# Performance work log

Hardware: AMD Instinct MI355X
Metric: run time of the kernel (lower is better)

## Reference

```python
import jax, jax.numpy as jnp
import numpy as np

H, D = 8, 16
HID = H * D  # 128 hidden channels
NU, NI = 20000, 50000
E_UI, E_IU, E_UU = 250000, 250000, 125000


def _agg(scores, vals, dst, n):
    # segment softmax over incoming edges per dst node, then scatter-add.
    # scores: [E, H], vals: [E, H, D], dst: [E]
    m = jax.ops.segment_max(scores, dst, num_segments=n)
    m = jnp.where(jnp.isfinite(m), m, 0.0)
    e = jnp.exp(scores - m[dst])
    den = jax.ops.segment_sum(e, dst, num_segments=n) + 1e-16
    alpha = e / den[dst]
    return jax.ops.segment_sum(vals * alpha[..., None], dst, num_segments=n)


def setup_inputs() -> dict:
    key = jax.random.key(0)
    ks = iter(jax.random.split(key, 40))
    def nrm(shape, scale):
        return jax.random.normal(next(ks), shape, dtype=jnp.float32) * scale
    L = 2
    inp = {}
    inp['x_user'] = nrm((NU, 128), 1.0)
    inp['x_item'] = nrm((NI, 64), 1.0)
    inp['edge_src_ui'] = jax.random.randint(next(ks), (E_UI,), 0, NU, dtype=jnp.int32)
    inp['edge_dst_ui'] = jax.random.randint(next(ks), (E_UI,), 0, NI, dtype=jnp.int32)
    inp['edge_src_iu'] = jax.random.randint(next(ks), (E_IU,), 0, NI, dtype=jnp.int32)
    inp['edge_dst_iu'] = jax.random.randint(next(ks), (E_IU,), 0, NU, dtype=jnp.int32)
    inp['edge_src_uu'] = jax.random.randint(next(ks), (E_UU,), 0, NU, dtype=jnp.int32)
    inp['edge_dst_uu'] = jax.random.randint(next(ks), (E_UU,), 0, NU, dtype=jnp.int32)
    inp['W_in_user'] = nrm((128, HID), 128 ** -0.5)
    inp['b_in_user'] = jnp.zeros((HID,), jnp.float32)
    inp['W_in_item'] = nrm((64, HID), 64 ** -0.5)
    inp['b_in_item'] = jnp.zeros((HID,), jnp.float32)
    inp['W_kqv_user'] = nrm((L, HID, 3 * HID), HID ** -0.5)
    inp['b_kqv_user'] = jnp.zeros((L, 3 * HID), jnp.float32)
    inp['W_kqv_item'] = nrm((L, HID, 3 * HID), HID ** -0.5)
    inp['b_kqv_item'] = jnp.zeros((L, 3 * HID), jnp.float32)
    inp['W_out_user'] = nrm((L, HID, HID), HID ** -0.5)
    inp['b_out_user'] = jnp.zeros((L, HID), jnp.float32)
    inp['W_out_item'] = nrm((L, HID, HID), HID ** -0.5)
    inp['b_out_item'] = jnp.zeros((L, HID), jnp.float32)
    inp['skip_user'] = jnp.ones((L,), jnp.float32)
    inp['skip_item'] = jnp.ones((L,), jnp.float32)
    inp['A_k'] = nrm((L, 3, H, D, D), D ** -0.5)
    inp['A_v'] = nrm((L, 3, H, D, D), D ** -0.5)
    inp['p_rel'] = jnp.ones((L, 3, H), jnp.float32)
    inp['W_lin'] = nrm((HID, 64), HID ** -0.5)
    inp['b_lin'] = jnp.zeros((64,), jnp.float32)
    return inp


def reference(x_user, x_item, edge_src_ui, edge_dst_ui, edge_src_iu, edge_dst_iu,
              edge_src_uu, edge_dst_uu, W_in_user, b_in_user, W_in_item, b_in_item,
              W_kqv_user, b_kqv_user, W_kqv_item, b_kqv_item, W_out_user, b_out_user,
              W_out_item, b_out_item, skip_user, skip_item, A_k, A_v, p_rel,
              W_lin, b_lin):
    inv_sqrt_d = 1.0 / jnp.sqrt(jnp.float32(D))
    # per-node-type input projection + relu
    xu = jax.nn.relu(x_user @ W_in_user + b_in_user)  # [NU, HID]
    xi = jax.nn.relu(x_item @ W_in_item + b_in_item)  # [NI, HID]
    L = W_kqv_user.shape[0]
    for l in range(L):
        kqv_u = xu @ W_kqv_user[l] + b_kqv_user[l]
        k_u, q_u, v_u = [t.reshape(-1, H, D) for t in jnp.split(kqv_u, 3, axis=1)]
        kqv_i = xi @ W_kqv_item[l] + b_kqv_item[l]
        k_i, q_i, v_i = [t.reshape(-1, H, D) for t in jnp.split(kqv_i, 3, axis=1)]

        def edge_msgs(k_src, v_src, q_dst, src, dst, r):
            # relation-specific key/value transforms, gathered per edge
            ke = jnp.einsum('ehd,hdf->ehf', k_src[src], A_k[l, r])  # [E,H,D]
            ve = jnp.einsum('ehd,hdf->ehf', v_src[src], A_v[l, r])  # [E,H,D]
            sc = (q_dst[dst] * ke).sum(-1) * p_rel[l, r] * inv_sqrt_d  # [E,H]
            return sc, ve

        s_ui, m_ui = edge_msgs(k_u, v_u, q_i, edge_src_ui, edge_dst_ui, 0)
        s_iu, m_iu = edge_msgs(k_i, v_i, q_u, edge_src_iu, edge_dst_iu, 1)
        s_uu, m_uu = edge_msgs(k_u, v_u, q_u, edge_src_uu, edge_dst_uu, 2)

        out_i = _agg(s_ui, m_ui, edge_dst_ui, NI).reshape(NI, HID)
        out_u = _agg(jnp.concatenate([s_iu, s_uu]),
                     jnp.concatenate([m_iu, m_uu]),
                     jnp.concatenate([edge_dst_iu, edge_dst_uu]), NU).reshape(NU, HID)

        # gelu -> per-type output linear -> sigmoid-gated skip (PyG HGTConv)
        a_u = jax.nn.gelu(out_u, approximate=False) @ W_out_user[l] + b_out_user[l]
        a_i = jax.nn.gelu(out_i, approximate=False) @ W_out_item[l] + b_out_item[l]
        g_u = jax.nn.sigmoid(skip_user[l])
        g_i = jax.nn.sigmoid(skip_item[l])
        xu = jax.nn.relu(g_u * a_u + (1.0 - g_u) * xu)
        xi = jax.nn.relu(g_i * a_i + (1.0 - g_i) * xi)
    # shared final linear over both node types; concat user then item rows
    out = jnp.concatenate([xu, xi], axis=0) @ W_lin + b_lin  # [NU+NI, 64]
    return out
```

## Files before the change

kernel.cpp:

```cpp
#include <hip/hip_runtime.h>
#include <math.h>

namespace {

constexpr int kNU  = 20000;
constexpr int kNI  = 50000;
constexpr int kEUI = 250000;
constexpr int kEIU = 250000;
constexpr int kEUU = 125000;
constexpr int kEU  = kEIU + kEUU;

typedef __attribute__((ext_vector_type(8))) short bf16x8_t;
typedef __attribute__((ext_vector_type(4))) float f32x4_t;

__device__ __forceinline__ float geluf(float x) {
  return 0.5f * x * (1.0f + erff(x * 0.7071067811865475f));
}

__device__ __forceinline__ void split_bf16(float x, unsigned short& hi, unsigned short& lo) {
  unsigned u = __float_as_uint(x);
  unsigned h = (u + 0x7FFFu + ((u >> 16) & 1u)) >> 16;
  hi = (unsigned short)h;
  float r = x - __uint_as_float(h << 16);
  unsigned ur = __float_as_uint(r);
  lo = (unsigned short)((ur + 0x7FFFu + ((ur >> 16) & 1u)) >> 16);
}

template <int ACT_IN, int EPI>
__global__ __launch_bounds__(256, 2) void mfma_gemm(
    const float* __restrict__ A, const unsigned short* __restrict__ Bt,
    const float* __restrict__ bias, float* C,
    int M, int N, int K,
    const float* x_old, const float* __restrict__ skip_scalar)
{
  __shared__ unsigned short sA[2][128][72];
  __shared__ unsigned short sB[2][128][72];
  const int tid = threadIdx.x;
  const int m0 = blockIdx.y * 128, n0 = blockIdx.x * 128;
  const int lane = tid & 63, w = tid >> 6;
  const int wm = w >> 1, wn = w & 1;
  const int fr = lane & 15, kg = lane >> 4;
  const unsigned short* Blo = Bt + (size_t)N * K;
  const int r = tid >> 1, seg = tid & 1;
  f32x4_t acc[4][4] = {};

  for (int k0 = 0; k0 < K; k0 += 64) {
    {
      const int arow = m0 + r;
      const bool am = arow < M;
      const float* ap = A + (size_t)arow * K + k0 + seg * 32;
      #pragma unroll
      for (int q = 0; q < 8; ++q) {
        float4 a = am ? *reinterpret_cast<const float4*>(ap + q * 4)
                      : make_float4(0.f, 0.f, 0.f, 0.f);
        if (ACT_IN == 1) { a.x = geluf(a.x); a.y = geluf(a.y); a.z = geluf(a.z); a.w = geluf(a.w); }
        ushort4 h, l;
        split_bf16(a.x, h.x, l.x); split_bf16(a.y, h.y, l.y);
        split_bf16(a.z, h.z, l.z); split_bf16(a.w, h.w, l.w);
        *reinterpret_cast<ushort4*>(&sA[0][r][seg * 32 + q * 4]) = h;
        *reinterpret_cast<ushort4*>(&sA[1][r][seg * 32 + q * 4]) = l;
      }
    }
    {
      const int brow = n0 + r;
      const bool bm = brow < N;
      const unsigned short* bh = Bt  + (size_t)brow * K + k0 + seg * 32;
      const unsigned short* bl = Blo + (size_t)brow * K + k0 + seg * 32;
      #pragma unroll
      for (int q = 0; q < 4; ++q) {
        uint4 vh = bm ? *reinterpret_cast<const uint4*>(bh + q * 8) : make_uint4(0, 0, 0, 0);
        uint4 vl = bm ? *reinterpret_cast<const uint4*>(bl + q * 8) : make_uint4(0, 0, 0, 0);
        *reinterpret_cast<uint4*>(&sB[0][r][seg * 32 + q * 8]) = vh;
        *reinterpret_cast<uint4*>(&sB[1][r][seg * 32 + q * 8]) = vl;
      }
    }
    __syncthreads();
    #pragma unroll
    for (int ks = 0; ks < 2; ++ks) {
      const int kb = ks * 32 + kg * 8;
      bf16x8_t ah[4], al[4], bh[4], bl[4];
      #pragma unroll
      for (int fm = 0; fm < 4; ++fm) {
        const int row = wm * 64 + fm * 16 + fr;
        ah[fm] = *reinterpret_cast<const bf16x8_t*>(&sA[0][row][kb]);
        al[fm] = *reinterpret_cast<const bf16x8_t*>(&sA[1][row][kb]);
      }
      #pragma unroll
      for (int fn = 0; fn < 4; ++fn) {
        const int row = wn * 64 + fn * 16 + fr;
        bh[fn] = *reinterpret_cast<const bf16x8_t*>(&sB[0][row][kb]);
        bl[fn] = *reinterpret_cast<const bf16x8_t*>(&sB[1][row][kb]);
      }
      #pragma unroll
      for (int fm = 0; fm < 4; ++fm)
        #pragma unroll
        for (int fn = 0; fn < 4; ++fn) {
          acc[fm][fn] = __builtin_amdgcn_mfma_f32_16x16x32_bf16(ah[fm], bh[fn], acc[fm][fn], 0, 0, 0);
          acc[fm][fn] = __builtin_amdgcn_mfma_f32_16x16x32_bf16(ah[fm], bl[fn], acc[fm][fn], 0, 0, 0);
          acc[fm][fn] = __builtin_amdgcn_mfma_f32_16x16x32_bf16(al[fm], bh[fn], acc[fm][fn], 0, 0, 0);
        }
    }
    __syncthreads();
  }

  float g = 0.f;
  if (EPI == 2) g = 1.f / (1.f + __expf(-skip_scalar[0]));
  #pragma unroll
  for (int fn = 0; fn < 4; ++fn) {
    const int col = n0 + wn * 64 + fn * 16 + fr;
    if (col >= N) continue;
    const float bv = bias[col];
    #pragma unroll
    for (int fm = 0; fm < 4; ++fm) {
      #pragma unroll
      for (int i = 0; i < 4; ++i) {
        const int row = m0 + wm * 64 + fm * 16 + kg * 4 + i;
        if (row >= M) continue;
        float v = acc[fm][fn][i] + bv;
        if (EPI == 1) v = fmaxf(v, 0.f);
        if (EPI == 2) {
          float xo = x_old[(size_t)row * 128 + col];
          v = fmaxf(g * v + (1.f - g) * xo, 0.f);
        }
        C[(size_t)row * N + col] = v;
      }
    }
  }
}

constexpr int kSlices = 16;

__device__ void conv_wt(const float* __restrict__ src, int ld, int cofs,
                        int Kd, int Nd, unsigned short* __restrict__ dst, int slice) {
  const int tot = Kd * Nd;
  for (int t = slice * 256 + threadIdx.x; t < tot; t += kSlices * 256) {
    const int n = t / Kd, k = t - n * Kd;
    unsigned short h, l;
    split_bf16(src[(size_t)k * ld + cofs + n], h, l);
    dst[t] = h; dst[tot + t] = l;
  }
}

__global__ __launch_bounds__(256) void build_weights(
    const float* __restrict__ Wku, const float* __restrict__ bku,
    const float* __restrict__ Wki, const float* __restrict__ bki,
    const float* __restrict__ A_k, const float* __restrict__ A_v,
    const float* __restrict__ p_rel,
    const float* __restrict__ W_in_u, const float* __restrict__ W_in_i,
    const float* __restrict__ W_out_u, const float* __restrict__ W_out_i,
    const float* __restrict__ W_lin,
    unsigned short* __restrict__ TWuU, unsigned short* __restrict__ TWiU,
    unsigned short* __restrict__ TWuI, unsigned short* __restrict__ TWqi,
    unsigned short* __restrict__ TWinU, unsigned short* __restrict__ TWinI,
    unsigned short* __restrict__ TWoutU, unsigned short* __restrict__ TWoutI,
    unsigned short* __restrict__ TWlin,
    float* __restrict__ buU, float* __restrict__ biU, float* __restrict__ buI)
{
  const int idx = blockIdx.x >> 4;
  const int slice = blockIdx.x & 15;
  if (idx < 12) {
    const int kv = idx & 1;
    const int lr = idx >> 1;
    const int l = lr / 3, r = lr - 3 * l;
    const float* A = (kv ? A_v : A_k) + (size_t)lr * 2048;
    const float* Wsrc = (r == 1) ? (Wki + (size_t)l * 128 * 384) : (Wku + (size_t)l * 128 * 384);
    const float* bsrc = (r == 1) ? (bki + (size_t)l * 384) : (bku + (size_t)l * 384);
    const int colsrc = kv ? 256 : 0;
    unsigned short* T; float* b; int colofs, Ntot;
    if (r == 2)      { T = TWuU + (size_t)l * 2 * 384 * 128; b = buU + l * 384; colofs = 128 + kv * 128; Ntot = 384; }
    else if (r == 1) { T = TWiU + (size_t)l * 2 * 256 * 128; b = biU + l * 256; colofs = kv * 128; Ntot = 256; }
    else             { T = TWuI + (size_t)l * 2 * 256 * 128; b = buI + l * 256; colofs = kv * 128; Ntot = 256; }
    __shared__ float sA[2048];
    for (int i = threadIdx.x; i < 2048; i += 256) sA[i] = A[i];
    __syncthreads();
    const int plane = Ntot * 128;
    for (int t = slice * 256 + threadIdx.x; t < 16384; t += kSlices * 256) {
      const int c = t >> 7, hf = t & 127, h = hf >> 4, f = hf & 15;
      const float scale = kv ? 1.f : p_rel[lr * 8 + h] * 0.25f;
      const float* wrow = Wsrc + (size_t)c * 384 + colsrc + h * 16;
      float s = 0.f;
      #pragma unroll
      for (int d = 0; d < 16; ++d) s += wrow[d] * sA[h * 256 + d * 16 + f];
      unsigned short hi, lo;
      split_bf16(s * scale, hi, lo);
      T[(size_t)(colofs + hf) * 128 + c] = hi;
      T[plane + (size_t)(colofs + hf) * 128 + c] = lo;
    }
    if (slice == 0) {
      for (int t = threadIdx.x; t < 128; t += 256) {
        const int h = t >> 4, f = t & 15;
        const float scale = kv ? 1.f : p_rel[lr * 8 + h] * 0.25f;
        float s = 0.f;
        #pragma unroll
        for (int d = 0; d < 16; ++d) s += bsrc[colsrc + h * 16 + d] * sA[h * 256 + d * 16 + f];
        b[colofs + t] = s * scale;
      }
    }
    return;
  }
  if (idx < 14) {
    const int l = idx - 12;
    const float* src = Wku + (size_t)l * 128 * 384;
    unsigned short* T = TWuU + (size_t)l * 2 * 384 * 128;
    const int plane = 384 * 128;
    for (int t = slice * 256 + threadIdx.x; t < 16384; t += kSlices * 256) {
      const int n = t >> 7, k = t & 127;
      unsigned short h, lo;
      split_bf16(src[(size_t)k * 384 + 128 + n], h, lo);
      T[(size_t)n * 128 + k] = h;
      T[plane + (size_t)n * 128 + k] = lo;
    }
    if (slice == 0)
      for (int t = threadIdx.x; t < 128; t += 256)
        buU[l * 384 + t] = bku[(size_t)l * 384 + 128 + t];
    return;
  }
  if (idx < 16) { conv_wt(Wki + (size_t)(idx - 14) * 128 * 384, 384, 128, 128, 128,
                          TWqi + (size_t)(idx - 14) * 2 * 128 * 128, slice); return; }
  if (idx == 16) { conv_wt(W_in_u, 128, 0, 128, 128, TWinU, slice); return; }
  if (idx == 17) { conv_wt(W_in_i, 128, 0, 64, 128, TWinI, slice); return; }
  if (idx < 20) { conv_wt(W_out_u + (size_t)(idx - 18) * 16384, 128, 0, 128, 128,
                          TWoutU + (size_t)(idx - 18) * 2 * 16384, slice); return; }
  if (idx < 22) { conv_wt(W_out_i + (size_t)(idx - 20) * 16384, 128, 0, 128, 128,
                          TWoutI + (size_t)(idx - 20) * 2 * 16384, slice); return; }
  conv_wt(W_lin, 64, 0, 128, 64, TWlin, slice);
}

__global__ void zero2_kernel(int* a, int na, int* b, int nb) {
  int i = blockIdx.x * 256 + threadIdx.x;
  if (i < na) a[i] = 0;
  if (i < nb) b[i] = 0;
}
__global__ void count_all(const int* __restrict__ dst_ui, const int* __restrict__ dst_iu,
                          const int* __restrict__ dst_uu,
                          int* __restrict__ cnt_i, int* __restrict__ cnt_u) {
  int e = blockIdx.x * 256 + threadIdx.x;
  if (e < kEUI) atomicAdd(&cnt_i[dst_ui[e]], 1);
  if (e < kEU) {
    int d = (e < kEIU) ? dst_iu[e] : dst_uu[e - kEIU];
    atomicAdd(&cnt_u[d], 1);
  }
}
__global__ void scatter_all(const int* __restrict__ dst_ui, const int* __restrict__ src_ui,
                            const int* __restrict__ dst_iu, const int* __restrict__ src_iu,
                            const int* __restrict__ dst_uu, const int* __restrict__ src_uu,
                            int* __restrict__ cur_i, int* __restrict__ list_i,
                            int* __restrict__ cur_u, int* __restrict__ list_u) {
  int e = blockIdx.x * 256 + threadIdx.x;
  if (e < kEUI) { int pos = atomicAdd(&cur_i[dst_ui[e]], 1); list_i[pos] = src_ui[e]; }
  if (e < kEU) {
    int d, sv;
    if (e < kEIU) { d = dst_iu[e]; sv = src_iu[e]; }
    else          { d = dst_uu[e - kEIU]; sv = src_uu[e - kEIU] | (int)0x80000000; }
    int pos = atomicAdd(&cur_u[d], 1);
    list_u[pos] = sv;
  }
}

__device__ void scan_body(const int* cnt_in, int* starts, int* cursor, int n) {
  __shared__ int wsum[16];
  __shared__ int s_carry;
  const int tid = threadIdx.x;
  const int lane = tid & 63, wv = tid >> 6;
  if (tid == 0) s_carry = 0;
  __syncthreads();
  for (int base = 0; base < n; base += 1024) {
    int i = base + tid;
    int v = (i < n) ? cnt_in[i] : 0;
    int s = v;
    #pragma unroll
    for (int off = 1; off < 64; off <<= 1) {
      int t = __shfl_up(s, off, 64);
      if (lane >= off) s += t;
    }
    if (lane == 63) wsum[wv] = s;
    __syncthreads();
    int woff = 0, total = 0;
    #pragma unroll
    for (int w = 0; w < 16; ++w) { total += wsum[w]; woff += (w < wv) ? wsum[w] : 0; }
    int excl = s_carry + woff + s - v;
    if (i < n) { starts[i] = excl; cursor[i] = excl; }
    __syncthreads();
    if (tid == 0) s_carry += total;
    __syncthreads();
  }
  if (tid == 0) starts[n] = s_carry;
}
__global__ __launch_bounds__(1024) void scan2_kernel(
    int* cnt_i, int* starts_i, int n_i, int* cnt_u, int* starts_u, int n_u) {
  if (blockIdx.x == 0) scan_body(cnt_i, starts_i, cnt_i, n_i);
  else                 scan_body(cnt_u, starts_u, cnt_u, n_u);
}

__global__ __launch_bounds__(256) void agg_wave_kernel(
    const int* __restrict__ starts, const int* __restrict__ list,
    const float* __restrict__ q, int qstride,
    const float* __restrict__ tabA, int strideA,
    const float* __restrict__ tabB, int strideB, int offB,
    float* __restrict__ out, int n_dst)
{
  const int dst = (int)((blockIdx.x * 256 + threadIdx.x) >> 6);
  if (dst >= n_dst) return;
  const int lane = threadIdx.x & 63;
  const int cofs = 2 * lane;
  const float2 qv = *reinterpret_cast<const float2*>(q + (size_t)dst * qstride + cofs);
  float m = -INFINITY, den = 0.f, a0 = 0.f, a1 = 0.f;
  const int i0 = starts[dst], i1 = starts[dst + 1];
  if (i0 < i1) {
    auto resolve = [&](int sv) -> const float* {
      return (sv < 0) ? tabB + (size_t)(sv & 0x7fffffff) * strideB + offB
                      : tabA + (size_t)sv * strideA;
    };
    int sv_n = list[i0];
    int sv_nn = (i0 + 1 < i1) ? list[i0 + 1] : 0;
    const float* kb = resolve(sv_n);
    float2 kk = *reinterpret_cast<const float2*>(kb + cofs);
    float2 vv = *reinterpret_cast<const float2*>(kb + 128 + cofs);
    for (int idx = i0; idx < i1; ++idx) {
      const float2 kc = kk, vc = vv;
      const int sv_next = sv_nn;
      if (idx + 2 < i1) sv_nn = list[idx + 2];
      if (idx + 1 < i1) {
        const float* kbn = resolve(sv_next);
        kk = *reinterpret_cast<const float2*>(kbn + cofs);
        vv = *reinterpret_cast<const float2*>(kbn + 128 + cofs);
      }
      float p = qv.x * kc.x + qv.y * kc.y;
      p += __shfl_xor(p, 1);
      p += __shfl_xor(p, 2);
      p += __shfl_xor(p, 4);
      const float mn = fmaxf(m, p);
      const float r  = __expf(m - mn);
      const float pe = __expf(p - mn);
      den = den * r + pe;
      a0  = a0 * r + pe * vc.x;
      a1  = a1 * r + pe * vc.y;
      m = mn;
    }
  }
  const float inv = 1.f / (den + 1e-16f);
  *reinterpret_cast<float2*>(out + (size_t)dst * 128 + cofs) = make_float2(a0 * inv, a1 * inv);
}

inline int cdiv(int a, int b) { return (a + b - 1) / b; }

}

extern "C" void kernel_launch(void* const* d_in, const int* in_sizes, int n_in,
                              void* d_out, int out_size, void* d_ws, size_t ws_size,
                              hipStream_t stream) {
  const float* x_user      = (const float*)d_in[0];
  const float* x_item      = (const float*)d_in[1];
  const int*   src_ui      = (const int*)d_in[2];
  const int*   dst_ui      = (const int*)d_in[3];
  const int*   src_iu      = (const int*)d_in[4];
  const int*   dst_iu      = (const int*)d_in[5];
  const int*   src_uu      = (const int*)d_in[6];
  const int*   dst_uu      = (const int*)d_in[7];
  const float* W_in_user   = (const float*)d_in[8];
  const float* b_in_user   = (const float*)d_in[9];
  const float* W_in_item   = (const float*)d_in[10];
  const float* b_in_item   = (const float*)d_in[11];
  const float* W_kqv_user  = (const float*)d_in[12];
  const float* b_kqv_user  = (const float*)d_in[13];
  const float* W_kqv_item  = (const float*)d_in[14];
  const float* b_kqv_item  = (const float*)d_in[15];
  const float* W_out_user  = (const float*)d_in[16];
  const float* b_out_user  = (const float*)d_in[17];
  const float* W_out_item  = (const float*)d_in[18];
  const float* b_out_item  = (const float*)d_in[19];
  const float* skip_user   = (const float*)d_in[20];
  const float* skip_item   = (const float*)d_in[21];
  const float* A_k         = (const float*)d_in[22];
  const float* A_v         = (const float*)d_in[23];
  const float* p_rel       = (const float*)d_in[24];
  const float* W_lin       = (const float*)d_in[25];
  const float* b_lin       = (const float*)d_in[26];
  float* out = (float*)d_out;
  (void)in_sizes; (void)n_in; (void)out_size; (void)ws_size;

  char* base = (char*)d_ws;
  size_t off = 0;
  auto alloc = [&](size_t nbytes) -> void* {
    void* p = base + off;
    off += (nbytes + 255) & ~(size_t)255;
    return p;
  };
  float* xu    = (float*)alloc((size_t)kNU * 128 * 4);
  float* xi    = (float*)alloc((size_t)kNI * 128 * 4);
  float* tab   = (float*)alloc((size_t)20480000 * 4);
  float* agg_u = (float*)alloc((size_t)kNU * 128 * 4);
  unsigned short* TWuU   = (unsigned short*)alloc((size_t)2 * 2 * 384 * 128 * 2);
  unsigned short* TWiU   = (unsigned short*)alloc((size_t)2 * 2 * 256 * 128 * 2);
  unsigned short* TWuI   = (unsigned short*)alloc((size_t)2 * 2 * 256 * 128 * 2);
  unsigned short* TWqi   = (unsigned short*)alloc((size_t)2 * 2 * 128 * 128 * 2);
  unsigned short* TWinU  = (unsigned short*)alloc((size_t)2 * 128 * 128 * 2);
  unsigned short* TWinI  = (unsigned short*)alloc((size_t)2 * 128 * 64 * 2);
  unsigned short* TWoutU = (unsigned short*)alloc((size_t)2 * 2 * 128 * 128 * 2);
  unsigned short* TWoutI = (unsigned short*)alloc((size_t)2 * 2 * 128 * 128 * 2);
  unsigned short* TWlin  = (unsigned short*)alloc((size_t)2 * 64 * 128 * 2);
  float* buU   = (float*)alloc((size_t)2 * 384 * 4);
  float* biU   = (float*)alloc((size_t)2 * 256 * 4);
  float* buI   = (float*)alloc((size_t)2 * 256 * 4);
  int* starts_i = (int*)alloc((size_t)(kNI + 1) * 4);
  int* cursor_i = (int*)alloc((size_t)kNI * 4);
  int* list_i   = (int*)alloc((size_t)kEUI * 4);
  int* starts_u = (int*)alloc((size_t)(kNU + 1) * 4);
  int* cursor_u = (int*)alloc((size_t)kNU * 4);
  int* list_u   = (int*)alloc((size_t)kEU * 4);

  float* u_all = tab + 0;
  float* i_all = tab + 7680000;
  float* u2    = tab + 0;
  float* q_i   = tab + 5120000;
  float* agg_i = tab + 11520000;

  zero2_kernel<<<cdiv(kNI, 256), 256, 0, stream>>>(cursor_i, kNI, cursor_u, kNU);
  count_all<<<cdiv(kEU, 256), 256, 0, stream>>>(dst_ui, dst_iu, dst_uu, cursor_i, cursor_u);
  scan2_kernel<<<2, 1024, 0, stream>>>(cursor_i, starts_i, kNI, cursor_u, starts_u, kNU);
  scatter_all<<<cdiv(kEU, 256), 256, 0, stream>>>(dst_ui, src_ui, dst_iu, src_iu,
                                                  dst_uu, src_uu, cursor_i, list_i,
                                                  cursor_u, list_u);

  build_weights<<<23 * kSlices, 256, 0, stream>>>(
      W_kqv_user, b_kqv_user, W_kqv_item, b_kqv_item, A_k, A_v, p_rel,
      W_in_user, W_in_item, W_out_user, W_out_item, W_lin,
      TWuU, TWiU, TWuI, TWqi, TWinU, TWinI, TWoutU, TWoutI, TWlin,
      buU, biU, buI);

  mfma_gemm<0, 1><<<dim3(1, cdiv(kNU, 128)), 256, 0, stream>>>(
      x_user, TWinU, b_in_user, xu, kNU, 128, 128, nullptr, nullptr);
  mfma_gemm<0, 1><<<dim3(1, cdiv(kNI, 128)), 256, 0, stream>>>(
      x_item, TWinI, b_in_item, xi, kNI, 128, 64, nullptr, nullptr);

  for (int l = 0; l < 2; ++l) {
    mfma_gemm<0, 0><<<dim3(3, cdiv(kNU, 128)), 256, 0, stream>>>(
        xu, TWuU + (size_t)l * 2 * 384 * 128, buU + l * 384, u_all, kNU, 384, 128,
        nullptr, nullptr);
    mfma_gemm<0, 0><<<dim3(2, cdiv(kNI, 128)), 256, 0, stream>>>(
        xi, TWiU + (size_t)l * 2 * 256 * 128, biU + l * 256, i_all, kNI, 256, 128,
        nullptr, nullptr);
    agg_wave_kernel<<<cdiv(kNU * 64, 256), 256, 0, stream>>>(
        starts_u, list_u, u_all, 384, i_all, 256, u_all, 384, 128, agg_u, kNU);

    mfma_gemm<0, 0><<<dim3(2, cdiv(kNU, 128)), 256, 0, stream>>>(
        xu, TWuI + (size_t)l * 2 * 256 * 128, buI + l * 256, u2, kNU, 256, 128,
        nullptr, nullptr);
    mfma_gemm<0, 0><<<dim3(1, cdiv(kNI, 128)), 256, 0, stream>>>(
        xi, TWqi + (size_t)l * 2 * 128 * 128, b_kqv_item + (size_t)l * 384 + 128,
        q_i, kNI, 128, 128, nullptr, nullptr);
    agg_wave_kernel<<<cdiv(kNI * 64, 256), 256, 0, stream>>>(
        starts_i, list_i, q_i, 128, u2, 256, u2, 256, 0, agg_i, kNI);

    mfma_gemm<1, 2><<<dim3(1, cdiv(kNU, 128)), 256, 0, stream>>>(
        agg_u, TWoutU + (size_t)l * 2 * 128 * 128, b_out_user + (size_t)l * 128,
        xu, kNU, 128, 128, xu, skip_user + l);
    mfma_gemm<1, 2><<<dim3(1, cdiv(kNI, 128)), 256, 0, stream>>>(
        agg_i, TWoutI + (size_t)l * 2 * 128 * 128, b_out_item + (size_t)l * 128,
        xi, kNI, 128, 128, xi, skip_item + l);
  }

  mfma_gemm<0, 0><<<dim3(1, cdiv(kNU + kNI, 128)), 256, 0, stream>>>(
      xu, TWlin, b_lin, out, kNU + kNI, 64, 128, nullptr, nullptr);
}
```

Before: 875.9 us.

## Store gathered key/value tables in fp16 and simplify aggregation loop

The GEMMs that produce per-edge key and value projections now write them as fp16 into packed tables, while query columns stay fp32. The aggregation kernel gathers half-precision k/v, halving the bytes per random gather, and converts to float for the online softmax. The software prefetch of the next row's k/v is removed in favour of a simpler loop that only prefetches the next index. Workspace layout is reshuffled to fit the smaller tables. The risks are fp16 rounding and range limits on k/v, and more exposed gather latency without the prefetch.

Measured after the change: 819.0 us. 6.5% less time.

```diff
diff --git a/kernel.cpp b/kernel.cpp
--- a/kernel.cpp
+++ b/kernel.cpp
@@ -12,6 +12,8 @@
 
 typedef __attribute__((ext_vector_type(8))) short bf16x8_t;
 typedef __attribute__((ext_vector_type(4))) float f32x4_t;
+
+struct h2v { _Float16 x, y; };
 
 __device__ __forceinline__ float geluf(float x) {
   return 0.5f * x * (1.0f + erff(x * 0.7071067811865475f));
@@ -26,12 +28,13 @@
   lo = (unsigned short)((ur + 0x7FFFu + ((ur >> 16) & 1u)) >> 16);
 }
 
-template <int ACT_IN, int EPI>
+template <int ACT_IN, int EPI, int OUT>
 __global__ __launch_bounds__(256, 2) void mfma_gemm(
     const float* __restrict__ A, const unsigned short* __restrict__ Bt,
     const float* __restrict__ bias, float* C,
     int M, int N, int K,
-    const float* x_old, const float* __restrict__ skip_scalar)
+    const float* x_old, const float* __restrict__ skip_scalar,
+    _Float16* __restrict__ Ckv, int qcols)
 {
   __shared__ unsigned short sA[2][128][72];
   __shared__ unsigned short sB[2][128][72];
@@ -105,6 +108,7 @@
 
   float g = 0.f;
   if (EPI == 2) g = 1.f / (1.f + __expf(-skip_scalar[0]));
+  const int kvN = (OUT == 1) ? (N - qcols) : 0;
   #pragma unroll
   for (int fn = 0; fn < 4; ++fn) {
     const int col = n0 + wn * 64 + fn * 16 + fr;
@@ -122,7 +126,12 @@
           float xo = x_old[(size_t)row * 128 + col];
           v = fmaxf(g * v + (1.f - g) * xo, 0.f);
         }
-        C[(size_t)row * N + col] = v;
+        if (OUT == 0) {
+          C[(size_t)row * N + col] = v;
+        } else {
+          if (col < qcols) C[(size_t)row * qcols + col] = v;
+          else             Ckv[(size_t)row * kvN + (col - qcols)] = (_Float16)v;
+        }
       }
     }
   }
@@ -294,49 +303,37 @@
 
 __global__ __launch_bounds__(256) void agg_wave_kernel(
     const int* __restrict__ starts, const int* __restrict__ list,
-    const float* __restrict__ q, int qstride,
-    const float* __restrict__ tabA, int strideA,
-    const float* __restrict__ tabB, int strideB, int offB,
+    const float* __restrict__ q,
+    const _Float16* __restrict__ tabA, const _Float16* __restrict__ tabB,
     float* __restrict__ out, int n_dst)
 {
   const int dst = (int)((blockIdx.x * 256 + threadIdx.x) >> 6);
   if (dst >= n_dst) return;
   const int lane = threadIdx.x & 63;
   const int cofs = 2 * lane;
-  const float2 qv = *reinterpret_cast<const float2*>(q + (size_t)dst * qstride + cofs);
+  const float2 qv = *reinterpret_cast<const float2*>(q + (size_t)dst * 128 + cofs);
   float m = -INFINITY, den = 0.f, a0 = 0.f, a1 = 0.f;
-  const int i0 = starts[dst], i1 = starts[dst + 1];
-  if (i0 < i1) {
-    auto resolve = [&](int sv) -> const float* {
-      return (sv < 0) ? tabB + (size_t)(sv & 0x7fffffff) * strideB + offB
-                      : tabA + (size_t)sv * strideA;
-    };
-    int sv_n = list[i0];
-    int sv_nn = (i0 + 1 < i1) ? list[i0 + 1] : 0;
-    const float* kb = resolve(sv_n);
-    float2 kk = *reinterpret_cast<const float2*>(kb + cofs);
-    float2 vv = *reinterpret_cast<const float2*>(kb + 128 + cofs);
-    for (int idx = i0; idx < i1; ++idx) {
-      const float2 kc = kk, vc = vv;
-      const int sv_next = sv_nn;
-      if (idx + 2 < i1) sv_nn = list[idx + 2];
-      if (idx + 1 < i1) {
-        const float* kbn = resolve(sv_next);
-        kk = *reinterpret_cast<const float2*>(kbn + cofs);
-        vv = *reinterpret_cast<const float2*>(kbn + 128 + cofs);
-      }
-      float p = qv.x * kc.x + qv.y * kc.y;
-      p += __shfl_xor(p, 1);
-      p += __shfl_xor(p, 2);
-      p += __shfl_xor(p, 4);
-      const float mn = fmaxf(m, p);
-      const float r  = __expf(m - mn);
-      const float pe = __expf(p - mn);
-      den = den * r + pe;
-      a0  = a0 * r + pe * vc.x;
-      a1  = a1 * r + pe * vc.y;
-      m = mn;
-    }
+  const int i1 = starts[dst + 1];
+  int idx = starts[dst];
+  int sv_next = (idx < i1) ? list[idx] : 0;
+  for (; idx < i1; ++idx) {
+    const int sv = sv_next;
+    if (idx + 1 < i1) sv_next = list[idx + 1];
+    const _Float16* kb = (sv < 0) ? tabB + (size_t)(sv & 0x7fffffff) * 256
+                                  : tabA + (size_t)sv * 256;
+    const h2v kk = *reinterpret_cast<const h2v*>(kb + cofs);
+    const h2v vv = *reinterpret_cast<const h2v*>(kb + 128 + cofs);
+    float p = qv.x * (float)kk.x + qv.y * (float)kk.y;
+    p += __shfl_xor(p, 1);
+    p += __shfl_xor(p, 2);
+    p += __shfl_xor(p, 4);
+    const float mn = fmaxf(m, p);
+    const float r  = __expf(m - mn);
+    const float pe = __expf(p - mn);
+    den = den * r + pe;
+    a0  = a0 * r + pe * (float)vv.x;
+    a1  = a1 * r + pe * (float)vv.y;
+    m = mn;
   }
   const float inv = 1.f / (den + 1e-16f);
   *reinterpret_cast<float2*>(out + (size_t)dst * 128 + cofs) = make_float2(a0 * inv, a1 * inv);
@@ -388,7 +385,7 @@
   };
   float* xu    = (float*)alloc((size_t)kNU * 128 * 4);
   float* xi    = (float*)alloc((size_t)kNI * 128 * 4);
-  float* tab   = (float*)alloc((size_t)20480000 * 4);
+  float* tab   = (float*)alloc((size_t)15360000 * 4);
   float* agg_u = (float*)alloc((size_t)kNU * 128 * 4);
   unsigned short* TWuU   = (unsigned short*)alloc((size_t)2 * 2 * 384 * 128 * 2);
   unsigned short* TWiU   = (unsigned short*)alloc((size_t)2 * 2 * 256 * 128 * 2);
@@ -409,11 +406,12 @@
   int* cursor_u = (int*)alloc((size_t)kNU * 4);
   int* list_u   = (int*)alloc((size_t)kEU * 4);
 
-  float* u_all = tab + 0;
-  float* i_all = tab + 7680000;
-  float* u2    = tab + 0;
-  float* q_i   = tab + 5120000;
-  float* agg_i = tab + 11520000;
+  float*    q_u   = tab + 0;
+  _Float16* u_kv2 = (_Float16*)(tab + 2560000);
+  _Float16* i_kv  = (_Float16*)(tab + 5120000);
+  _Float16* u_kv0 = (_Float16*)(tab + 0);
+  float*    q_i   = tab + 2560000;
+  float*    agg_i = tab + 8960000;
 
   zero2_kernel<<<cdiv(kNI, 256), 256, 0, stream>>>(cursor_i, kNI, cursor_u, kNU);
   count_all<<<cdiv(kEU, 256), 256, 0, stream>>>(dst_ui, dst_iu, dst_uu, cursor_i, cursor_u);
@@ -428,38 +426,38 @@
       TWuU, TWiU, TWuI, TWqi, TWinU, TWinI, TWoutU, TWoutI, TWlin,
       buU, biU, buI);
 
-  mfma_gemm<0, 1><<<dim3(1, cdiv(kNU, 128)), 256, 0, stream>>>(
-      x_user, TWinU, b_in_user, xu, kNU, 128, 128, nullptr, nullptr);
-  mfma_gemm<0, 1><<<dim3(1, cdiv(kNI, 128)), 256, 0, stream>>>(
-      x_item, TWinI, b_in_item, xi, kNI, 128, 64, nullptr, nullptr);
+  mfma_gemm<0, 1, 0><<<dim3(1, cdiv(kNU, 128)), 256, 0, stream>>>(
+      x_user, TWinU, b_in_user, xu, kNU, 128, 128, nullptr, nullptr, nullptr, 0);
+  mfma_gemm<0, 1, 0><<<dim3(1, cdiv(kNI, 128)), 256, 0, stream>>>(
+      x_item, TWinI, b_in_item, xi, kNI, 128, 64, nullptr, nullptr, nullptr, 0);
 
   for (int l = 0; l < 2; ++l) {
-    mfma_gemm<0, 0><<<dim3(3, cdiv(kNU, 128)), 256, 0, stream>>>(
-        xu, TWuU + (size_t)l * 2 * 384 * 128, buU + l * 384, u_all, kNU, 384, 128,
-        nullptr, nullptr);
-    mfma_gemm<0, 0><<<dim3(2, cdiv(kNI, 128)), 256, 0, stream>>>(
-        xi, TWiU + (size_t)l * 2 * 256 * 128, biU + l * 256, i_all, kNI, 256, 128,
-        nullptr, nullptr);
+    mfma_gemm<0, 0, 1><<<dim3(3, cdiv(kNU, 128)), 256, 0, stream>>>(
+        xu, TWuU + (size_t)l * 2 * 384 * 128, buU + l * 384, q_u, kNU, 384, 128,
+        nullptr, nullptr, u_kv2, 128);
+    mfma_gemm<0, 0, 1><<<dim3(2, cdiv(kNI, 128)), 256, 0, stream>>>(
+        xi, TWiU + (size_t)l * 2 * 256 * 128, biU + l * 256, nullptr, kNI, 256, 128,
+        nullptr, nullptr, i_kv, 0);
     agg_wave_kernel<<<cdiv(kNU * 64, 256), 256, 0, stream>>>(
-        starts_u, list_u, u_all, 384, i_all, 256, u_all, 384, 128, agg_u, kNU);
-
-    mfma_gemm<0, 0><<<dim3(2, cdiv(kNU, 128)), 256, 0, stream>>>(
-        xu, TWuI + (size_t)l * 2 * 256 * 128, buI + l * 256, u2, kNU, 256, 128,
-        nullptr, nullptr);
-    mfma_gemm<0, 0><<<dim3(1, cdiv(kNI, 128)), 256, 0, stream>>>(
+        starts_u, list_u, q_u, i_kv, u_kv2, agg_u, kNU);
+
+    mfma_gemm<0, 0, 1><<<dim3(2, cdiv(kNU, 128)), 256, 0, stream>>>(
+        xu, TWuI + (size_t)l * 2 * 256 * 128, buI + l * 256, nullptr, kNU, 256, 128,
+        nullptr, nullptr, u_kv0, 0);
+    mfma_gemm<0, 0, 0><<<dim3(1, cdiv(kNI, 128)), 256, 0, stream>>>(
         xi, TWqi + (size_t)l * 2 * 128 * 128, b_kqv_item + (size_t)l * 384 + 128,
-        q_i, kNI, 128, 128, nullptr, nullptr);
+        q_i, kNI, 128, 128, nullptr, nullptr, nullptr, 0);
     agg_wave_kernel<<<cdiv(kNI * 64, 256), 256, 0, stream>>>(
-        starts_i, list_i, q_i, 128, u2, 256, u2, 256, 0, agg_i, kNI);
-
-    mfma_gemm<1, 2><<<dim3(1, cdiv(kNU, 128)), 256, 0, stream>>>(
+        starts_i, list_i, q_i, u_kv0, u_kv0, agg_i, kNI);
+
+    mfma_gemm<1, 2, 0><<<dim3(1, cdiv(kNU, 128)), 256, 0, stream>>>(
         agg_u, TWoutU + (size_t)l * 2 * 128 * 128, b_out_user + (size_t)l * 128,
-        xu, kNU, 128, 128, xu, skip_user + l);
-    mfma_gemm<1, 2><<<dim3(1, cdiv(kNI, 128)), 256, 0, stream>>>(
+        xu, kNU, 128, 128, xu, skip_user + l, nullptr, 0);
+    mfma_gemm<1, 2, 0><<<dim3(1, cdiv(kNI, 128)), 256, 0, stream>>>(
         agg_i, TWoutI + (size_t)l * 2 * 128 * 128, b_out_item + (size_t)l * 128,
-        xi, kNI, 128, 128, xi, skip_item + l);
-  }
-
-  mfma_gemm<0, 0><<<dim3(1, cdiv(kNU + kNI, 128)), 256, 0, stream>>>(
-      xu, TWlin, b_lin, out, kNU + kNI, 64, 128, nullptr, nullptr);
-}
+        xi, kNI, 128, 128, xi, skip_item + l, nullptr, 0);
+  }
+
+  mfma_gemm<0, 0, 0><<<dim3(1, cdiv(kNU + kNI, 128)), 256, 0, stream>>>(
+      xu, TWlin, b_lin, out, kNU + kNI, 64, 128, nullptr, nullptr, nullptr, 0);
+}
```
